# Kernel tuning notes

Hardware: AMD Instinct MI355X
Metric: run time of the kernel (lower is better)

## Reference

```python
import jax, jax.numpy as jnp
import numpy as np

N_HEADS = 16
D_HEAD = 64
D_MODEL = 1024


def setup_inputs() -> dict:
    key = jax.random.key(0)
    k_x, k_q, k_k, k_v, k_o = jax.random.split(key, 5)
    std = 1.0 / np.sqrt(D_MODEL)
    B, T = 4, 2048
    return {
        "x": jax.random.normal(k_x, (B, T, D_MODEL), dtype=jnp.float32),
        "W_Q": jax.random.normal(k_q, (D_MODEL, N_HEADS * D_HEAD), dtype=jnp.float32) * std,
        "W_K": jax.random.normal(k_k, (D_MODEL, N_HEADS * D_HEAD), dtype=jnp.float32) * std,
        "W_V": jax.random.normal(k_v, (D_MODEL, N_HEADS * D_HEAD), dtype=jnp.float32) * std,
        "W_O": jax.random.normal(k_o, (N_HEADS * D_HEAD, D_MODEL), dtype=jnp.float32) * std,
    }


def reference(x, W_Q, W_K, W_V, W_O):
    B, T, _ = x.shape
    H, D = N_HEADS, D_HEAD
    # projections: [B,T,H,D]
    q = (x @ W_Q).reshape(B, T, H, D)
    k = (x @ W_K).reshape(B, T, H, D)
    v = (x @ W_V).reshape(B, T, H, D)
    scale = 1.0 / jnp.sqrt(jnp.asarray(D, dtype=x.dtype))
    # scores: [B,H,T,T]
    scores = jnp.einsum("bqhd,bkhd->bhqk", q, k) * scale
    causal = jnp.tril(jnp.ones((T, T), dtype=bool))
    scores = jnp.where(causal[None, None], scores, jnp.asarray(-jnp.inf, dtype=scores.dtype))
    attn = jax.nn.softmax(scores, axis=-1)
    out = jnp.einsum("bhqk,bkhd->bqhd", attn, v).reshape(B, T, H * D)
    return out @ W_O
```

## Files before the change

### kernel.cpp

```cpp
#include <hip/hip_runtime.h>

typedef unsigned short u16;
typedef short bf16x8 __attribute__((ext_vector_type(8)));
typedef float f32x4 __attribute__((ext_vector_type(4)));

__device__ inline u16 f32_to_bf16(float f) {
  union { float f; unsigned int u; } v; v.f = f;
  unsigned int r = v.u + 0x7FFFu + ((v.u >> 16) & 1u);
  return (u16)(r >> 16);
}

__device__ inline float red16_sum(float x) {
#pragma unroll
  for (int m = 8; m >= 1; m >>= 1) x += __shfl_xor(x, m);
  return x;
}

__device__ __forceinline__ void gl_lds16(const u16* g, u16* l) {
  __builtin_amdgcn_global_load_lds(
      (const __attribute__((address_space(1))) void*)g,
      (__attribute__((address_space(3))) void*)l, 16, 0, 0);
}

__global__ __launch_bounds__(256) void xcvt_kernel(const float* __restrict__ in,
                                                   u16* __restrict__ out) {
  size_t i = (size_t)blockIdx.x * 256 + threadIdx.x;
  float4 f0 = ((const float4*)in)[2 * i];
  float4 f1 = ((const float4*)in)[2 * i + 1];
  union { u16 t[8]; uint4 v; } pk;
  pk.t[0] = f32_to_bf16(f0.x); pk.t[1] = f32_to_bf16(f0.y);
  pk.t[2] = f32_to_bf16(f0.z); pk.t[3] = f32_to_bf16(f0.w);
  pk.t[4] = f32_to_bf16(f1.x); pk.t[5] = f32_to_bf16(f1.y);
  pk.t[6] = f32_to_bf16(f1.z); pk.t[7] = f32_to_bf16(f1.w);
  ((uint4*)out)[i] = pk.v;
}

__global__ __launch_bounds__(256) void transpose_cvt4_kernel(const float* __restrict__ i0,
                                                             const float* __restrict__ i1,
                                                             const float* __restrict__ i2,
                                                             const float* __restrict__ i3,
                                                             u16* __restrict__ wbase) {
  const int z = blockIdx.z;
  const float* in = (z == 0) ? i0 : (z == 1) ? i1 : (z == 2) ? i2 : i3;
  u16* out = wbase + (size_t)z * (1 << 20);
  __shared__ __align__(16) float tile[32][33];
  const int tx = threadIdx.x & 31, ty = threadIdx.x >> 5;
  const int bx = blockIdx.x * 32, by = blockIdx.y * 32;
#pragma unroll
  for (int i = 0; i < 32; i += 8)
    tile[ty + i][tx] = in[(size_t)(by + ty + i) * 1024 + bx + tx];
  __syncthreads();
#pragma unroll
  for (int i = 0; i < 32; i += 8)
    out[(size_t)(bx + ty + i) * 1024 + by + tx] = f32_to_bf16(tile[tx][ty + i]);
}


#define QKV_BAR asm volatile("s_barrier" ::: "memory")
#define QKV_VMW(n) asm volatile("s_waitcnt vmcnt(" #n ")" ::: "memory")
#define QKV_LGK0 asm volatile("s_waitcnt lgkmcnt(0)" ::: "memory")
#define SCHED0 __builtin_amdgcn_sched_barrier(0)

#define DSR(dst, addr, off) \
  asm volatile("ds_read_b128 %0, %1 offset:" #off : "=v"(dst) : "v"(addr))

#define LDA_MH0(ad) { DSR(afr[0], ad, 0);    DSR(afr[1], ad, 1024); \
                      DSR(afr[2], ad, 2048); DSR(afr[3], ad, 3072); }
#define LDA_MH1(ad) { DSR(afr[0], ad, 4096); DSR(afr[1], ad, 5120); \
                      DSR(afr[2], ad, 6144); DSR(afr[3], ad, 7168); }
#define LDB_ALL(bd) { DSR(bfr[0], bd, 0);    DSR(bfr[1], bd, 1024); \
                      DSR(bfr[2], bd, 2048); DSR(bfr[3], bd, 3072); }

#define STAGE_A(d2, kh, kt) do {                                   \
    const u16* _p = A + aSrc + (size_t)(kt) * 64 + (kh) * 32;      \
    gl_lds16(_p, &sA[d2][kh][dstOff]);                             \
    gl_lds16(_p + 16 * 1024, &sA[d2][kh][dstOff + 512]);           \
  } while (0)
#define STAGE_B(d2, kh, kt) do {                                   \
    const u16* _p = Bt + bSrc + (size_t)(kt) * 64 + (kh) * 32;     \
    gl_lds16(_p, &sB[d2][kh][dstOff]);                             \
    gl_lds16(_p + 16 * 1024, &sB[d2][kh][dstOff + 512]);           \
  } while (0)
#define MMA(mh) {                                                  \
    _Pragma("unroll") for (int mt = 0; mt < 4; ++mt)               \
      _Pragma("unroll") for (int nt = 0; nt < 4; ++nt)             \
        acc[(mh) * 4 + mt][nt] = __builtin_amdgcn_mfma_f32_16x16x32_bf16( \
            afr[mt], bfr[nt], acc[(mh) * 4 + mt][nt], 0, 0, 0); }

__global__ __launch_bounds__(512, 2) void gemm_qkv_kernel(const u16* __restrict__ A,
                                                          const u16* __restrict__ Bt,
                                                          u16* __restrict__ Q,
                                                          u16* __restrict__ K,
                                                          u16* __restrict__ Vt) {
  __shared__ __align__(16) u16 sA[2][2][256 * 32];
  __shared__ __align__(16) u16 sB[2][2][256 * 32];

  const int tid = threadIdx.x;
  const int lane = tid & 63, wave = tid >> 6;
  const int quad = lane >> 4, l16 = lane & 15;

  const int lin = blockIdx.y * 12 + blockIdx.x;
  const int swz = (lin & 7) * 48 + (lin >> 3);
  const int bn = swz % 12, bm = swz / 12;
  const int m0 = bm * 256, n0 = bn * 256;
  const int wm = (wave >> 2) * 128, wn = (wave & 3) * 64;

  const int sRow = lane >> 2;
  const int sGrp = (lane & 3) ^ ((lane >> 3) & 3);
  const size_t aSrc = (size_t)(m0 + wave * 32 + sRow) * 1024 + sGrp * 8;
  const size_t bSrc = (size_t)(n0 + wave * 32 + sRow) * 1024 + sGrp * 8;
  const int dstOff = wave * 1024;

  const int swr = (quad ^ ((l16 >> 1) & 3)) * 8;
  const int aOff = (wm + l16) * 32 + swr;
  const int bOff = (wn + l16) * 32 + swr;

  const unsigned aRd = (unsigned)(size_t)&sA[0][0][0] + (unsigned)aOff * 2u;
  const unsigned bRd = (unsigned)(size_t)&sB[0][0][0] + (unsigned)bOff * 2u;

  f32x4 acc[8][4] = {};
  bf16x8 afr[4], bfr[4];

  STAGE_A(0, 0, 0); STAGE_B(0, 0, 0); STAGE_A(0, 1, 0); STAGE_B(0, 1, 0);
  QKV_VMW(0);
  QKV_BAR;

  for (int t = 0; t < 16; ++t) {
    const int d = t & 1, dn = d ^ 1;
    const bool pf = (t < 15);
    const unsigned a0 = aRd + (unsigned)(d * 32768);
    const unsigned b0 = bRd + (unsigned)(d * 32768);

    if (pf) { STAGE_A(dn, 0, t + 1); STAGE_B(dn, 0, t + 1); }
    LDB_ALL(b0); LDA_MH0(a0);
    QKV_LGK0;
    SCHED0;
    __builtin_amdgcn_s_setprio(1);
    MMA(0);
    __builtin_amdgcn_s_setprio(0);
    SCHED0;
    LDA_MH1(a0);
    QKV_LGK0;
    SCHED0;
    __builtin_amdgcn_s_setprio(1);
    MMA(1);
    __builtin_amdgcn_s_setprio(0);
    SCHED0;

    if (pf) { STAGE_A(dn, 1, t + 1); STAGE_B(dn, 1, t + 1); }
    LDB_ALL(b0 + 16384u); LDA_MH0(a0 + 16384u);
    QKV_LGK0;
    SCHED0;
    __builtin_amdgcn_s_setprio(1);
    MMA(0);
    __builtin_amdgcn_s_setprio(0);
    SCHED0;
    LDA_MH1(a0 + 16384u);
    QKV_LGK0;
    SCHED0;
    __builtin_amdgcn_s_setprio(1);
    MMA(1);
    __builtin_amdgcn_s_setprio(0);
    SCHED0;

    QKV_VMW(0);
    QKV_BAR;
  }

  const int proj = bn >> 2;
#pragma unroll
  for (int mi = 0; mi < 8; ++mi) {
#pragma unroll
    for (int nt = 0; nt < 4; ++nt) {
#pragma unroll
      for (int r = 0; r < 4; ++r) {
        int mrow = m0 + wm + mi * 16 + quad * 4 + r;
        int nloc = (n0 & 1023) + wn + nt * 16 + l16;
        u16 bv = f32_to_bf16(acc[mi][nt][r]);
        if (proj == 0) {
          Q[(size_t)mrow * 1024 + nloc] = bv;
        } else if (proj == 1) {
          K[(size_t)mrow * 1024 + nloc] = bv;
        } else {
          int b = mrow >> 11, tt = mrow & 2047;
          int h = nloc >> 6, dd = nloc & 63;
          Vt[((size_t)((b * 16 + h) * 64 + dd)) * 2048 + tt] = bv;
        }
      }
    }
  }
}

#undef STAGE_A
#undef STAGE_B
#undef MMA

__global__ __launch_bounds__(256) void gemm_out_kernel(const u16* __restrict__ A,
                                                       const u16* __restrict__ Bt,
                                                       float* __restrict__ C) {
  __shared__ u16 sA[128 * 64];
  __shared__ u16 sB[128 * 64];

  const int tid = threadIdx.x;
  const int lane = tid & 63, wave = tid >> 6;
  const int quad = lane >> 4, l16 = lane & 15;
  const int bn = blockIdx.x, bm = blockIdx.y;
  const int m0 = bm * 128, n0 = bn * 128;
  const int wm = (wave >> 1) * 64, wn = (wave & 1) * 64;

  const int lr = lane >> 3;
  const int gsw = (lane & 7) ^ (lr & 7);
  const int sw0 = ((0 * 4 + quad) ^ (l16 & 7)) * 8;
  const int sw1 = ((1 * 4 + quad) ^ (l16 & 7)) * 8;

  f32x4 acc[4][4] = {};

  for (int k0 = 0; k0 < 1024; k0 += 64) {
    __syncthreads();
#pragma unroll
    for (int i = 0; i < 4; ++i) {
      int c = wave * 4 + i;
      int row = c * 8 + lr;
      gl_lds16(A + (size_t)(m0 + row) * 1024 + k0 + gsw * 8, sA + c * 512);
      gl_lds16(Bt + (size_t)(n0 + row) * 1024 + k0 + gsw * 8, sB + c * 512);
    }
    __syncthreads();

#pragma unroll
    for (int kk = 0; kk < 2; ++kk) {
      const int sw = kk ? sw1 : sw0;
      bf16x8 afr[4], bfr[4];
#pragma unroll
      for (int mt = 0; mt < 4; ++mt)
        afr[mt] = *(const bf16x8*)(sA + (wm + mt * 16 + l16) * 64 + sw);
#pragma unroll
      for (int nt = 0; nt < 4; ++nt)
        bfr[nt] = *(const bf16x8*)(sB + (wn + nt * 16 + l16) * 64 + sw);
#pragma unroll
      for (int mt = 0; mt < 4; ++mt)
#pragma unroll
        for (int nt = 0; nt < 4; ++nt)
          acc[mt][nt] = __builtin_amdgcn_mfma_f32_16x16x32_bf16(afr[mt], bfr[nt],
                                                                acc[mt][nt], 0, 0, 0);
    }
  }

#pragma unroll
  for (int mt = 0; mt < 4; ++mt)
#pragma unroll
    for (int nt = 0; nt < 4; ++nt)
#pragma unroll
      for (int r = 0; r < 4; ++r) {
        int mrow = m0 + wm + mt * 16 + quad * 4 + r;
        int ncol = n0 + wn + nt * 16 + l16;
        C[(size_t)mrow * 1024 + ncol] = acc[mt][nt][r];
      }
}

#define LDS_S 72

__global__ __launch_bounds__(256, 4) void attn_kernel(const u16* __restrict__ Qm,
                                                      const u16* __restrict__ Km,
                                                      const u16* __restrict__ Vt,
                                                      u16* __restrict__ Ctx) {
  const int pi = blockIdx.x;
  const int h = blockIdx.y, b = blockIdx.z;
  const int tid = threadIdx.x, lane = tid & 63, wave = tid >> 6;
  const int quad = lane >> 4, l16 = lane & 15;
  const int q64[2] = {pi, 31 - pi};

  __shared__ __align__(16) u16 sK[64 * LDS_S];
  __shared__ __align__(16) u16 sV[64 * LDS_S];
  __shared__ __align__(16) u16 sP[4][2][16 * LDS_S];

  bf16x8 qf[2][2];
#pragma unroll
  for (int s = 0; s < 2; ++s) {
    const size_t qrow = (size_t)(b * 2048 + q64[s] * 64 + wave * 16 + l16);
#pragma unroll
    for (int kk = 0; kk < 2; ++kk)
      qf[s][kk] = *(const bf16x8*)(Qm + qrow * 1024 + h * 64 + kk * 32 + quad * 8);
  }

  f32x4 o_acc[2][4] = {};
  float ps[2][4] = {};

  const int nkt = 32 - pi;
  for (int kt = 0; kt < nkt; ++kt) {
    const int k0 = kt * 64;
    __syncthreads();
#pragma unroll
    for (int i = 0; i < 2; ++i) {
      int c = tid + 256 * i;
      int row = c >> 3, col = (c & 7) * 8;
      *(uint4*)(sK + row * LDS_S + col) =
          *(const uint4*)(Km + ((size_t)(b * 2048 + k0 + row)) * 1024 + h * 64 + col);
      *(uint4*)(sV + row * LDS_S + col) =
          *(const uint4*)(Vt + ((size_t)((b * 16 + h) * 64 + row)) * 2048 + k0 + col);
    }
    __syncthreads();

#pragma unroll
    for (int s = 0; s < 2; ++s) {
      const int qmin = q64[s] * 64 + wave * 16;
      if (k0 > qmin + 15) continue;

      f32x4 sc[4];
#pragma unroll
      for (int nt = 0; nt < 4; ++nt) {
        f32x4 a = {};
#pragma unroll
        for (int kk = 0; kk < 2; ++kk) {
          bf16x8 kf = *(const bf16x8*)(sK + (nt * 16 + l16) * LDS_S + kk * 32 + quad * 8);
          a = __builtin_amdgcn_mfma_f32_16x16x32_bf16(qf[s][kk], kf, a, 0, 0, 0);
        }
        sc[nt] = a;
      }

      const bool need_mask = (k0 + 63) > qmin;
#pragma unroll
      for (int nt = 0; nt < 4; ++nt) {
#pragma unroll
        for (int r = 0; r < 4; ++r) {
          float v = sc[nt][r] * 0.125f;
          if (need_mask) {
            int qi = qmin + quad * 4 + r;
            int kj = k0 + nt * 16 + l16;
            if (kj > qi) v = -1e30f;
          }
          float p = __expf(v);
          sc[nt][r] = p;
          ps[s][r] += p;
        }
      }

#pragma unroll
      for (int nt = 0; nt < 4; ++nt)
#pragma unroll
        for (int r = 0; r < 4; ++r)
          sP[wave][s][(quad * 4 + r) * LDS_S + nt * 16 + l16] = f32_to_bf16(sc[nt][r]);

#pragma unroll
      for (int kk = 0; kk < 2; ++kk) {
        bf16x8 pf = *(const bf16x8*)(sP[wave][s] + l16 * LDS_S + kk * 32 + quad * 8);
#pragma unroll
        for (int dt = 0; dt < 4; ++dt) {
          bf16x8 vf = *(const bf16x8*)(sV + (dt * 16 + l16) * LDS_S + kk * 32 + quad * 8);
          o_acc[s][dt] = __builtin_amdgcn_mfma_f32_16x16x32_bf16(pf, vf,
                                                                 o_acc[s][dt], 0, 0, 0);
        }
      }
    }
  }

  float inv_l[2][4];
#pragma unroll
  for (int s = 0; s < 2; ++s)
#pragma unroll
    for (int r = 0; r < 4; ++r)
      inv_l[s][r] = 1.0f / red16_sum(ps[s][r]);

#pragma unroll
  for (int s = 0; s < 2; ++s)
#pragma unroll
    for (int dt = 0; dt < 4; ++dt)
#pragma unroll
      for (int r = 0; r < 4; ++r) {
        int trow = q64[s] * 64 + wave * 16 + quad * 4 + r;
        Ctx[((size_t)(b * 2048 + trow)) * 1024 + h * 64 + dt * 16 + l16] =
            f32_to_bf16(o_acc[s][dt][r] * inv_l[s][r]);
      }
}

extern "C" void kernel_launch(void* const* d_in, const int* in_sizes, int n_in,
                              void* d_out, int out_size, void* d_ws, size_t ws_size,
                              hipStream_t stream) {
  const float* x  = (const float*)d_in[0];
  const float* wq = (const float*)d_in[1];
  const float* wk = (const float*)d_in[2];
  const float* wv = (const float*)d_in[3];
  const float* wo = (const float*)d_in[4];
  u16* ws = (u16*)d_ws;

  u16* wtqkv = ws;
  u16* wto  = ws + 3 * (size_t)(1 << 20);
  u16* Q    = ws + 4 * (size_t)(1 << 20);
  u16* K    = ws + 12 * (size_t)(1 << 20);
  u16* Vt   = ws + 20 * (size_t)(1 << 20);
  u16* Ctx  = ws + 28 * (size_t)(1 << 20);
  u16* xb   = Ctx;
  float* out = (float*)d_out;

  dim3 tb(256);
  xcvt_kernel<<<dim3(4096), tb, 0, stream>>>(x, xb);
  transpose_cvt4_kernel<<<dim3(32, 32, 4), tb, 0, stream>>>(wq, wk, wv, wo, ws);

  gemm_qkv_kernel<<<dim3(12, 32), dim3(512), 0, stream>>>(xb, wtqkv, Q, K, Vt);

  attn_kernel<<<dim3(16, 16, 4), tb, 0, stream>>>(Q, K, Vt, Ctx);

  gemm_out_kernel<<<dim3(8, 64), tb, 0, stream>>>(Ctx, wto, out);
}
```

Before: 286.9 us.

## Retile QKV GEMM to 256x192 tiles for better CU occupancy

Changes the QKV projection GEMM tile from 256x256 to 256x192, so the grid grows from 384 to 512 blocks. With 256 CUs and two blocks per CU, that fills exactly one wave of blocks instead of leaving some CUs idle. The B operand now uses a 64-wide K row in LDS with a new swizzle and staging pattern, and the epilogue picks Q/K/V per 16-column subtile because tiles can straddle projection boundaries. Each wave does a 128x48 subtile, which gives lower MFMA density per LDS read of A.

```diff
diff --git a/kernel.cpp b/kernel.cpp
--- a/kernel.cpp
+++ b/kernel.cpp
@@ -68,22 +68,19 @@
                       DSR(afr[2], ad, 2048); DSR(afr[3], ad, 3072); }
 #define LDA_MH1(ad) { DSR(afr[0], ad, 4096); DSR(afr[1], ad, 5120); \
                       DSR(afr[2], ad, 6144); DSR(afr[3], ad, 7168); }
-#define LDB_ALL(bd) { DSR(bfr[0], bd, 0);    DSR(bfr[1], bd, 1024); \
-                      DSR(bfr[2], bd, 2048); DSR(bfr[3], bd, 3072); }
-
-#define STAGE_A(d2, kh, kt) do {                                   \
-    const u16* _p = A + aSrc + (size_t)(kt) * 64 + (kh) * 32;      \
-    gl_lds16(_p, &sA[d2][kh][dstOff]);                             \
-    gl_lds16(_p + 16 * 1024, &sA[d2][kh][dstOff + 512]);           \
+#define LDB3(bd) { DSR(bfr[0], bd, 0); DSR(bfr[1], bd, 2048); DSR(bfr[2], bd, 4096); }
+
+#define STAGE_A(d2, kh, kt) do {                                       \
+    const u16* _p = A + aSrc + (size_t)(kt) * 64 + (kh) * 32;          \
+    gl_lds16(_p, sAf + (d2) * 16384 + (kh) * 8192 + wave * 1024);      \
+    gl_lds16(_p + 16 * 1024, sAf + (d2) * 16384 + (kh) * 8192 + wave * 1024 + 512); \
   } while (0)
-#define STAGE_B(d2, kh, kt) do {                                   \
-    const u16* _p = Bt + bSrc + (size_t)(kt) * 64 + (kh) * 32;     \
-    gl_lds16(_p, &sB[d2][kh][dstOff]);                             \
-    gl_lds16(_p + 16 * 1024, &sB[d2][kh][dstOff + 512]);           \
-  } while (0)
-#define MMA(mh) {                                                  \
-    _Pragma("unroll") for (int mt = 0; mt < 4; ++mt)               \
-      _Pragma("unroll") for (int nt = 0; nt < 4; ++nt)             \
+#define STAGE_B(d2, kt, j)                                             \
+    gl_lds16(Bt + bSrc + (size_t)(kt) * 64 + (j) * 8192,               \
+             sBf + (d2) * 12288 + (wave * 3 + (j)) * 512)
+#define MMA(mh) {                                                      \
+    _Pragma("unroll") for (int mt = 0; mt < 4; ++mt)                   \
+      _Pragma("unroll") for (int nt = 0; nt < 3; ++nt)                 \
         acc[(mh) * 4 + mt][nt] = __builtin_amdgcn_mfma_f32_16x16x32_bf16( \
             afr[mt], bfr[nt], acc[(mh) * 4 + mt][nt], 0, 0, 0); }
 
@@ -92,36 +89,33 @@
                                                           u16* __restrict__ Q,
                                                           u16* __restrict__ K,
                                                           u16* __restrict__ Vt) {
-  __shared__ __align__(16) u16 sA[2][2][256 * 32];
-  __shared__ __align__(16) u16 sB[2][2][256 * 32];
+  __shared__ __align__(16) u16 sAf[2 * 2 * 256 * 32];
+  __shared__ __align__(16) u16 sBf[2 * 192 * 64];
 
   const int tid = threadIdx.x;
   const int lane = tid & 63, wave = tid >> 6;
   const int quad = lane >> 4, l16 = lane & 15;
 
-  const int lin = blockIdx.y * 12 + blockIdx.x;
-  const int swz = (lin & 7) * 48 + (lin >> 3);
-  const int bn = swz % 12, bm = swz / 12;
-  const int m0 = bm * 256, n0 = bn * 256;
-  const int wm = (wave >> 2) * 128, wn = (wave & 3) * 64;
-
-  const int sRow = lane >> 2;
-  const int sGrp = (lane & 3) ^ ((lane >> 3) & 3);
-  const size_t aSrc = (size_t)(m0 + wave * 32 + sRow) * 1024 + sGrp * 8;
-  const size_t bSrc = (size_t)(n0 + wave * 32 + sRow) * 1024 + sGrp * 8;
-  const int dstOff = wave * 1024;
-
-  const int swr = (quad ^ ((l16 >> 1) & 3)) * 8;
-  const int aOff = (wm + l16) * 32 + swr;
-  const int bOff = (wn + l16) * 32 + swr;
-
-  const unsigned aRd = (unsigned)(size_t)&sA[0][0][0] + (unsigned)aOff * 2u;
-  const unsigned bRd = (unsigned)(size_t)&sB[0][0][0] + (unsigned)bOff * 2u;
-
-  f32x4 acc[8][4] = {};
-  bf16x8 afr[4], bfr[4];
-
-  STAGE_A(0, 0, 0); STAGE_B(0, 0, 0); STAGE_A(0, 1, 0); STAGE_B(0, 1, 0);
+  const int lin = blockIdx.y * 16 + blockIdx.x;
+  const int swz = (lin & 7) * 64 + (lin >> 3);
+  const int bn = swz & 15, bm = swz >> 4;
+  const int m0 = bm * 256, n0 = bn * 192;
+  const int wm = (wave >> 2) * 128, wn = (wave & 3) * 48;
+
+  const size_t aSrc = (size_t)(m0 + wave * 32 + (lane >> 2)) * 1024 +
+                      (size_t)(((lane & 3) ^ ((lane >> 3) & 3)) * 8);
+  const size_t bSrc = (size_t)(n0 + wave * 24 + (lane >> 3)) * 1024 +
+                      (size_t)(((lane & 4) | ((lane & 3) ^ ((lane >> 4) & 3))) * 8);
+
+  const int rsw = (quad ^ ((l16 >> 1) & 3)) * 16;
+  const unsigned aRd = (unsigned)(size_t)sAf + (unsigned)((wm + l16) * 64 + rsw);
+  const unsigned bRd = (unsigned)(size_t)sBf + (unsigned)((wn + l16) * 128 + rsw);
+
+  f32x4 acc[8][3] = {};
+  bf16x8 afr[4], bfr[3];
+
+  STAGE_A(0, 0, 0); STAGE_B(0, 0, 0); STAGE_B(0, 0, 1); STAGE_B(0, 0, 2);
+  STAGE_A(0, 1, 0);
   QKV_VMW(0);
   QKV_BAR;
 
@@ -129,10 +123,10 @@
     const int d = t & 1, dn = d ^ 1;
     const bool pf = (t < 15);
     const unsigned a0 = aRd + (unsigned)(d * 32768);
-    const unsigned b0 = bRd + (unsigned)(d * 32768);
-
-    if (pf) { STAGE_A(dn, 0, t + 1); STAGE_B(dn, 0, t + 1); }
-    LDB_ALL(b0); LDA_MH0(a0);
+    const unsigned b0 = bRd + (unsigned)(d * 24576);
+
+    if (pf) { STAGE_A(dn, 0, t + 1); STAGE_B(dn, t + 1, 0); }
+    LDB3(b0); LDA_MH0(a0);
     QKV_LGK0;
     SCHED0;
     __builtin_amdgcn_s_setprio(1);
@@ -147,8 +141,8 @@
     __builtin_amdgcn_s_setprio(0);
     SCHED0;
 
-    if (pf) { STAGE_A(dn, 1, t + 1); STAGE_B(dn, 1, t + 1); }
-    LDB_ALL(b0 + 16384u); LDA_MH0(a0 + 16384u);
+    if (pf) { STAGE_A(dn, 1, t + 1); STAGE_B(dn, t + 1, 1); STAGE_B(dn, t + 1, 2); }
+    LDB3(b0 + 64u); LDA_MH0(a0 + 16384u);
     QKV_LGK0;
     SCHED0;
     __builtin_amdgcn_s_setprio(1);
@@ -167,19 +161,20 @@
     QKV_BAR;
   }
 
-  const int proj = bn >> 2;
 #pragma unroll
   for (int mi = 0; mi < 8; ++mi) {
 #pragma unroll
-    for (int nt = 0; nt < 4; ++nt) {
+    for (int nt = 0; nt < 3; ++nt) {
+      const int ngb = n0 + wn + nt * 16;
+      const int pr = ngb >> 10;
+      const int nloc = (ngb & 1023) + l16;
 #pragma unroll
       for (int r = 0; r < 4; ++r) {
         int mrow = m0 + wm + mi * 16 + quad * 4 + r;
-        int nloc = (n0 & 1023) + wn + nt * 16 + l16;
         u16 bv = f32_to_bf16(acc[mi][nt][r]);
-        if (proj == 0) {
+        if (pr == 0) {
           Q[(size_t)mrow * 1024 + nloc] = bv;
-        } else if (proj == 1) {
+        } else if (pr == 1) {
           K[(size_t)mrow * 1024 + nloc] = bv;
         } else {
           int b = mrow >> 11, tt = mrow & 2047;
@@ -395,7 +390,7 @@
   xcvt_kernel<<<dim3(4096), tb, 0, stream>>>(x, xb);
   transpose_cvt4_kernel<<<dim3(32, 32, 4), tb, 0, stream>>>(wq, wk, wv, wo, ws);
 
-  gemm_qkv_kernel<<<dim3(12, 32), dim3(512), 0, stream>>>(xb, wtqkv, Q, K, Vt);
+  gemm_qkv_kernel<<<dim3(16, 32), dim3(512), 0, stream>>>(xb, wtqkv, Q, K, Vt);
 
   attn_kernel<<<dim3(16, 16, 4), tb, 0, stream>>>(Q, K, Vt, Ctx);
 
```

Result: no change. 290.0 us (+1.1%).

## Double-buffer output projection GEMM with 128x256 tiles and swizzled block order

Applied to the files above, without the earlier changes.

Rewrites the output projection GEMM so that each 512-thread block computes a 128x256 tile. Global-to-LDS loads go into a double buffer split into K halves, so the next tile's loads are issued while MFMAs run on the current one. Blocks are remapped in a swizzled order to improve L2 reuse, and MFMA sections run at raised wave priority. It reuses the QKV kernel's wait, barrier and LDS-read macros, which adds coupling and register pressure and leaves fewer blocks in flight for this small GEMM.

```diff
diff --git a/kernel.cpp b/kernel.cpp
--- a/kernel.cpp
+++ b/kernel.cpp
@@ -195,54 +195,83 @@
 #undef STAGE_B
 #undef MMA
 
-__global__ __launch_bounds__(256) void gemm_out_kernel(const u16* __restrict__ A,
-                                                       const u16* __restrict__ Bt,
-                                                       float* __restrict__ C) {
-  __shared__ u16 sA[128 * 64];
-  __shared__ u16 sB[128 * 64];
+
+#define OSTAGE_A(d2, kh, kt)                                            \
+    gl_lds16(A + aSrc + (size_t)(kt) * 64 + (kh) * 32,                  \
+             &sA[d2][kh][wave * 512])
+#define OSTAGE_B(d2, kh, kt) do {                                       \
+    const u16* _p = Bt + bSrc + (size_t)(kt) * 64 + (kh) * 32;          \
+    gl_lds16(_p, &sB[d2][kh][wave * 1024]);                             \
+    gl_lds16(_p + 16 * 1024, &sB[d2][kh][wave * 1024 + 512]);           \
+  } while (0)
+#define LDA_ALL(ad) { DSR(afr[0], ad, 0);    DSR(afr[1], ad, 1024); \
+                      DSR(afr[2], ad, 2048); DSR(afr[3], ad, 3072); }
+#define OMMA {                                                          \
+    _Pragma("unroll") for (int mt = 0; mt < 4; ++mt)                    \
+      _Pragma("unroll") for (int nt = 0; nt < 4; ++nt)                  \
+        acc[mt][nt] = __builtin_amdgcn_mfma_f32_16x16x32_bf16(          \
+            afr[mt], bfr[nt], acc[mt][nt], 0, 0, 0); }
+
+__global__ __launch_bounds__(512, 2) void gemm_out_kernel(const u16* __restrict__ A,
+                                                          const u16* __restrict__ Bt,
+                                                          float* __restrict__ C) {
+  __shared__ __align__(16) u16 sA[2][2][128 * 32];
+  __shared__ __align__(16) u16 sB[2][2][256 * 32];
 
   const int tid = threadIdx.x;
   const int lane = tid & 63, wave = tid >> 6;
   const int quad = lane >> 4, l16 = lane & 15;
-  const int bn = blockIdx.x, bm = blockIdx.y;
-  const int m0 = bm * 128, n0 = bn * 128;
-  const int wm = (wave >> 1) * 64, wn = (wave & 1) * 64;
-
-  const int lr = lane >> 3;
-  const int gsw = (lane & 7) ^ (lr & 7);
-  const int sw0 = ((0 * 4 + quad) ^ (l16 & 7)) * 8;
-  const int sw1 = ((1 * 4 + quad) ^ (l16 & 7)) * 8;
+
+  const int lin = blockIdx.y * 4 + blockIdx.x;
+  const int swz = (lin & 7) * 32 + (lin >> 3);
+  const int bn = swz & 3, bm = swz >> 2;
+  const int m0 = bm * 128, n0 = bn * 256;
+  const int wm = (wave >> 2) * 64, wn = (wave & 3) * 64;
+
+  const int sRow = lane >> 2;
+  const int sGrp = (lane & 3) ^ ((lane >> 3) & 3);
+  const size_t aSrc = (size_t)(m0 + wave * 16 + sRow) * 1024 + sGrp * 8;
+  const size_t bSrc = (size_t)(n0 + wave * 32 + sRow) * 1024 + sGrp * 8;
+
+  const int swr = (quad ^ ((l16 >> 1) & 3)) * 8;
+  const unsigned aRd = (unsigned)(size_t)&sA[0][0][0] +
+                       (unsigned)(((wm + l16) * 32 + swr) * 2);
+  const unsigned bRd = (unsigned)(size_t)&sB[0][0][0] +
+                       (unsigned)(((wn + l16) * 32 + swr) * 2);
 
   f32x4 acc[4][4] = {};
-
-  for (int k0 = 0; k0 < 1024; k0 += 64) {
-    __syncthreads();
-#pragma unroll
-    for (int i = 0; i < 4; ++i) {
-      int c = wave * 4 + i;
-      int row = c * 8 + lr;
-      gl_lds16(A + (size_t)(m0 + row) * 1024 + k0 + gsw * 8, sA + c * 512);
-      gl_lds16(Bt + (size_t)(n0 + row) * 1024 + k0 + gsw * 8, sB + c * 512);
-    }
-    __syncthreads();
-
-#pragma unroll
-    for (int kk = 0; kk < 2; ++kk) {
-      const int sw = kk ? sw1 : sw0;
-      bf16x8 afr[4], bfr[4];
-#pragma unroll
-      for (int mt = 0; mt < 4; ++mt)
-        afr[mt] = *(const bf16x8*)(sA + (wm + mt * 16 + l16) * 64 + sw);
-#pragma unroll
-      for (int nt = 0; nt < 4; ++nt)
-        bfr[nt] = *(const bf16x8*)(sB + (wn + nt * 16 + l16) * 64 + sw);
-#pragma unroll
-      for (int mt = 0; mt < 4; ++mt)
-#pragma unroll
-        for (int nt = 0; nt < 4; ++nt)
-          acc[mt][nt] = __builtin_amdgcn_mfma_f32_16x16x32_bf16(afr[mt], bfr[nt],
-                                                                acc[mt][nt], 0, 0, 0);
-    }
+  bf16x8 afr[4], bfr[4];
+
+  OSTAGE_A(0, 0, 0); OSTAGE_B(0, 0, 0); OSTAGE_A(0, 1, 0); OSTAGE_B(0, 1, 0);
+  QKV_VMW(0);
+  QKV_BAR;
+
+  for (int t = 0; t < 16; ++t) {
+    const int d = t & 1, dn = d ^ 1;
+    const bool pf = (t < 15);
+    const unsigned a0 = aRd + (unsigned)(d * 16384);
+    const unsigned b0 = bRd + (unsigned)(d * 32768);
+
+    if (pf) { OSTAGE_A(dn, 0, t + 1); OSTAGE_B(dn, 0, t + 1); }
+    LDB_ALL(b0); LDA_ALL(a0);
+    QKV_LGK0;
+    SCHED0;
+    __builtin_amdgcn_s_setprio(1);
+    OMMA;
+    __builtin_amdgcn_s_setprio(0);
+    SCHED0;
+
+    if (pf) { OSTAGE_A(dn, 1, t + 1); OSTAGE_B(dn, 1, t + 1); }
+    LDB_ALL(b0 + 16384u); LDA_ALL(a0 + 8192u);
+    QKV_LGK0;
+    SCHED0;
+    __builtin_amdgcn_s_setprio(1);
+    OMMA;
+    __builtin_amdgcn_s_setprio(0);
+    SCHED0;
+
+    QKV_VMW(0);
+    QKV_BAR;
   }
 
 #pragma unroll
@@ -256,6 +285,11 @@
         C[(size_t)mrow * 1024 + ncol] = acc[mt][nt][r];
       }
 }
+
+#undef OSTAGE_A
+#undef OSTAGE_B
+#undef LDA_ALL
+#undef OMMA
 
 #define LDS_S 72
 
@@ -399,5 +433,5 @@
 
   attn_kernel<<<dim3(16, 16, 4), tb, 0, stream>>>(Q, K, Vt, Ctx);
 
-  gemm_out_kernel<<<dim3(8, 64), tb, 0, stream>>>(Ctx, wto, out);
-}
+  gemm_out_kernel<<<dim3(4, 64), dim3(512), 0, stream>>>(Ctx, wto, out);
+}
```

Measured after the change: 285.3 us. No clear change (-0.5%).
